# Kernel optimization log

Hardware: AMD Instinct MI355X
Metric: run time of the kernel (lower is better)

The kernel has to match this reference:

```python
import jax, jax.numpy as jnp
import numpy as np

B, S, D, H, F = 16, 1024, 256, 8, 1024
HD = D // H  # head_dim = 32
EPS = 1e-5


def setup_inputs() -> dict:
    key = jax.random.key(0)
    ks = jax.random.split(key, 12)
    sc = 0.02
    return {
        "x":      jax.random.normal(ks[0], (B, S, D), dtype=jnp.float32),
        "gamma1": jnp.ones((S, D), dtype=jnp.float32),
        "beta1":  jnp.zeros((S, D), dtype=jnp.float32),
        "Wqkv":   jax.random.normal(ks[1], (3 * D, D), dtype=jnp.float32) * sc,
        "bqkv":   jnp.zeros((3 * D,), dtype=jnp.float32),
        "Wo":     jax.random.normal(ks[2], (D, D), dtype=jnp.float32) * sc,
        "bo":     jnp.zeros((D,), dtype=jnp.float32),
        "gamma2": jnp.ones((S, D), dtype=jnp.float32),
        "beta2":  jnp.zeros((S, D), dtype=jnp.float32),
        "W1":     jax.random.normal(ks[3], (F, D), dtype=jnp.float32) * sc,
        "b1":     jnp.zeros((F,), dtype=jnp.float32),
        "W2":     jax.random.normal(ks[4], (D, F), dtype=jnp.float32) * sc,
        "b2":     jnp.zeros((D,), dtype=jnp.float32),
    }


def _layernorm_2d(x, gamma, beta):
    # normalizes jointly over the last TWO dims (seq, d_model), biased variance
    mean = jnp.mean(x, axis=(-2, -1), keepdims=True)
    var = jnp.mean((x - mean) ** 2, axis=(-2, -1), keepdims=True)
    y = (x - mean) / jnp.sqrt(var + EPS)
    return gamma * y + beta


def _mha(x, Wqkv, bqkv, Wo, bo):
    b, s, d = x.shape
    qkv = x @ Wqkv.T + bqkv                                  # [B,S,3D]
    qkv = qkv.reshape(b, s, H, 3 * HD).transpose(0, 2, 1, 3)  # [B,H,S,3HD]
    q, k, v = jnp.split(qkv, 3, axis=-1)                      # each [B,H,S,HD]
    scores = jnp.einsum("bhqd,bhkd->bhqk", q, k) / np.sqrt(HD).astype(np.float32)
    attn = jax.nn.softmax(scores, axis=-1)                    # [B,H,S,S]
    values = jnp.einsum("bhqk,bhkd->bhqd", attn, v)           # [B,H,S,HD]
    # NOTE: original torch code reshapes (B,H,S,HD)->(B,S,H*HD) WITHOUT permuting
    # back; we faithfully reproduce that (row-major reshape, same as torch).
    values = values.reshape(b, s, H * HD)
    return values @ Wo.T + bo


def reference(x, gamma1, beta1, Wqkv, bqkv, Wo, bo, gamma2, beta2, W1, b1, W2, b2):
    # pre-norm attention block (dropout is identity at inference)
    h = _layernorm_2d(x, gamma1, beta1)
    h = _mha(h, Wqkv, bqkv, Wo, bo)
    x = x + h
    # pre-norm MLP block
    h = _layernorm_2d(x, gamma2, beta2)
    h = jax.nn.relu(h @ W1.T + b1) @ W2.T + b2
    return x + h
```

## Files before the change

kernel.cpp:

```cpp
#include <hip/hip_runtime.h>
#include <cstdint>
#include <cstddef>

#define SDn (1024*256)

typedef unsigned short u16;
typedef unsigned int   u32;
typedef __bf16 bf16x8 __attribute__((ext_vector_type(8)));
typedef u16    u16x4v __attribute__((ext_vector_type(4)));
typedef u32    u32x4v __attribute__((ext_vector_type(4)));
typedef float  f32x4  __attribute__((ext_vector_type(4)));
typedef float  f32x16 __attribute__((ext_vector_type(16)));

__device__ __forceinline__ u16 f2bf(float f){
  u32 u = __builtin_bit_cast(u32, f);
  u32 r = u + 0x7FFFu + ((u >> 16) & 1u);
  return (u16)(r >> 16);
}

#if __has_builtin(__builtin_amdgcn_exp2f)
#define EXP2(x) __builtin_amdgcn_exp2f(x)
#else
#define EXP2(x) exp2f(x)
#endif

__device__ __forceinline__ u32 cvtpk(float a, float b){
  u32 r;
  asm("v_cvt_pk_bf16_f32 %0, %1, %2" : "=v"(r) : "v"(a), "v"(b));
  return r;
}

__device__ __forceinline__ void gll16(const void* g, void* l){
  __builtin_amdgcn_global_load_lds((const __attribute__((address_space(1))) void*)g,
                                   (__attribute__((address_space(3))) void*)l, 16, 0, 0);
}

__global__ void castw(const float* __restrict__ w0, const float* __restrict__ w1,
                      const float* __restrict__ w2, const float* __restrict__ w3,
                      u16* __restrict__ o0, u16* __restrict__ o1,
                      u16* __restrict__ o2, u16* __restrict__ o3)
{
  int i = blockIdx.x * 256 + threadIdx.x;
  const float* src; u16* dst; int j = i;
  if      (j <  49152){ src = w0; dst = o0; }
  else if (j <  65536){ src = w1; dst = o1; j -=  49152; }
  else if (j < 131072){ src = w2; dst = o2; j -=  65536; }
  else               { src = w3; dst = o3; j -= 131072; }
  float4 v = ((const float4*)src)[j];
  u16x4v o; o[0]=f2bf(v.x); o[1]=f2bf(v.y); o[2]=f2bf(v.z); o[3]=f2bf(v.w);
  ((u16x4v*)dst)[j] = o;
}

__global__ void ln_partial(const float* __restrict__ x, float2* __restrict__ part)
{
  int b = blockIdx.y, c = blockIdx.x, t = threadIdx.x;
  const float4* p = (const float4*)(x + (size_t)b*SDn + (size_t)c*4096);
  float s = 0.f, q = 0.f;
  #pragma unroll
  for (int i=0;i<4;i++){
    float4 v = p[t + i*256];
    s += v.x+v.y+v.z+v.w;
    q += v.x*v.x + v.y*v.y + v.z*v.z + v.w*v.w;
  }
  #pragma unroll
  for (int o=32;o;o>>=1){ s += __shfl_down(s,o); q += __shfl_down(q,o); }
  __shared__ float2 red[4];
  if ((t & 63) == 0) red[t>>6] = make_float2(s,q);
  __syncthreads();
  if (t == 0){
    float S=0.f,Q=0.f;
    #pragma unroll
    for (int i=0;i<4;i++){ S += red[i].x; Q += red[i].y; }
    part[b*64 + c] = make_float2(S,Q);
  }
}

__global__ void ln_apply(const float* __restrict__ x, const float* __restrict__ gamma,
                         const float* __restrict__ beta, const float2* __restrict__ part,
                         u16* __restrict__ y)
{
  int b = blockIdx.y, c = blockIdx.x, t = threadIdx.x;
  __shared__ float2 stat;
  if (t < 64){
    float2 v = part[b*64 + t];
    float s = v.x, q = v.y;
    #pragma unroll
    for (int o=32;o;o>>=1){ s += __shfl_down(s,o); q += __shfl_down(q,o); }
    if (t == 0){
      float mean = s / (float)SDn;
      float var  = q / (float)SDn - mean*mean;
      stat = make_float2(mean, rsqrtf(var + 1e-5f));
    }
  }
  __syncthreads();
  const float mean = stat.x, rstd = stat.y;
  const size_t off = (size_t)b*SDn + (size_t)c*4096;
  const float4* px = (const float4*)(x + off);
  const float4* pg = (const float4*)(gamma + (size_t)c*4096);
  const float4* pb = (const float4*)(beta  + (size_t)c*4096);
  u16x4v* py = (u16x4v*)(y + off);
  #pragma unroll
  for (int i=0;i<4;i++){
    float4 xv = px[t + i*256];
    float4 gv = pg[t + i*256];
    float4 bv = pb[t + i*256];
    u16x4v o;
    o[0] = f2bf(gv.x*(xv.x-mean)*rstd + bv.x);
    o[1] = f2bf(gv.y*(xv.y-mean)*rstd + bv.y);
    o[2] = f2bf(gv.z*(xv.z-mean)*rstd + bv.z);
    o[3] = f2bf(gv.w*(xv.w-mean)*rstd + bv.w);
    py[t + i*256] = o;
  }
}

template<int EPI>
__launch_bounds__(256, 4)
__global__ void gemm128(const u16* __restrict__ A, const u16* __restrict__ W,
                        const float* __restrict__ bias,
                        u16* __restrict__ o0, u16* __restrict__ o1, u16* __restrict__ o2,
                        int K, int N)
{
  __shared__ u16 As[2][4096];
  __shared__ u16 Bs[2][4096];
  const int tid  = threadIdx.x;
  const int lane = tid & 63;
  const int wid  = tid >> 6;
  const int wm = wid >> 1, wn = wid & 1;
  const int g  = lane >> 4;
  const int lr = lane & 15;
  const int m0 = blockIdx.x * 128;
  const int n0 = blockIdx.y * 128;

  f32x4 zf = {0.f,0.f,0.f,0.f};
  f32x4 acc[4][4];
  #pragma unroll
  for (int i=0;i<4;i++)
    #pragma unroll
    for (int j=0;j<4;j++) acc[i][j] = zf;

  const int r0 = tid >> 2, c0 = tid & 3;
  const int cs = c0 ^ ((r0 >> 1) & 3);
  const u16* Ar0 = A + (size_t)(m0 + r0     )*K + cs*8;
  const u16* Ar1 = A + (size_t)(m0 + r0 + 64)*K + cs*8;
  const u16* Wr0 = W + (size_t)(n0 + r0     )*K + cs*8;
  const u16* Wr1 = W + (size_t)(n0 + r0 + 64)*K + cs*8;

  int aoff[4], boff[4];
  #pragma unroll
  for (int m=0;m<4;m++){
    int ra = wm*64 + m*16 + lr;
    aoff[m] = (ra*4 + (g ^ ((ra>>1)&3))) * 8;
    int rb = wn*64 + m*16 + lr;
    boff[m] = (rb*4 + (g ^ ((rb>>1)&3))) * 8;
  }

  auto STAGE = [&](int buf, int k0){
    gll16(Ar0 + k0, &As[buf][tid*8]);
    gll16(Ar1 + k0, &As[buf][(tid+256)*8]);
    gll16(Wr0 + k0, &Bs[buf][tid*8]);
    gll16(Wr1 + k0, &Bs[buf][(tid+256)*8]);
  };

  STAGE(0, 0);
  __syncthreads();
  int cur = 0;
  for (int k0 = 0; k0 < K; k0 += 32){
    if (k0 + 32 < K) STAGE(cur^1, k0 + 32);
    bf16x8 af[4], bfv[4];
    #pragma unroll
    for (int m=0;m<4;m++) af[m]  = *(const bf16x8*)(&As[cur][aoff[m]]);
    #pragma unroll
    for (int n=0;n<4;n++) bfv[n] = *(const bf16x8*)(&Bs[cur][boff[n]]);
    #pragma unroll
    for (int m=0;m<4;m++)
      #pragma unroll
      for (int n=0;n<4;n++)
        acc[m][n] = __builtin_amdgcn_mfma_f32_16x16x32_bf16(af[m], bfv[n], acc[m][n], 0, 0, 0);
    __syncthreads();
    cur ^= 1;
  }

  #pragma unroll
  for (int m=0;m<4;m++){
    const int rowb = m0 + wm*64 + m*16 + g*4;
    #pragma unroll
    for (int n=0;n<4;n++){
      const int col = n0 + wn*64 + n*16 + lr;
      const float bc = bias[col];
      if constexpr (EPI == 0){
        const int hh  = col / 96;
        const int rem = col - hh*96;
        const int which = rem >> 5;
        const int d = rem & 31;
        #pragma unroll
        for (int rr=0;rr<4;rr++){
          const int rw = rowb + rr;
          const int b = rw >> 10, s = rw & 1023;
          float v = acc[m][n][rr] + bc;
          if (which == 0)
            o0[((size_t)((b*8 + hh)*1024 + s))*32 + d] = f2bf(v * (0.17677669529663689f * 1.4426950408889634f));
          else if (which == 1)
            o1[((size_t)((b*8 + hh)*1024 + s))*32 + d] = f2bf(v);
          else
            o2[((size_t)((b*8 + hh)*32 + d))*1024 + s] = f2bf(v);
        }
      } else {
        #pragma unroll
        for (int rr=0;rr<4;rr++){
          float v = acc[m][n][rr] + bc;
          o0[(size_t)(rowb + rr) * N + col] = f2bf(v > 0.f ? v : 0.f);
        }
      }
    }
  }
}

__launch_bounds__(256, 4)
__global__ void gemm64(const u16* __restrict__ A, const u16* __restrict__ W,
                       const float* __restrict__ bias, const float* __restrict__ res,
                       float* __restrict__ outF, int K, int N)
{
  __shared__ u16 As[2][2048];
  __shared__ u16 Bs[2][4096];
  const int tid  = threadIdx.x;
  const int lane = tid & 63;
  const int wid  = tid >> 6;
  const int g  = lane >> 4;
  const int lr = lane & 15;
  const int m0 = blockIdx.x * 64;
  const int n0 = blockIdx.y * 128;

  f32x4 zf = {0.f,0.f,0.f,0.f};
  f32x4 acc[4][2];
  #pragma unroll
  for (int i=0;i<4;i++){ acc[i][0]=zf; acc[i][1]=zf; }

  const int r0 = tid >> 2, c0 = tid & 3;
  const int cs = c0 ^ ((r0 >> 1) & 3);
  const u16* Asrc  = A + (size_t)(m0 + r0)*K + cs*8;
  const u16* Wsrc0 = W + (size_t)(n0 + r0     )*K + cs*8;
  const u16* Wsrc1 = W + (size_t)(n0 + r0 + 64)*K + cs*8;

  int aoff[4], boff[2];
  #pragma unroll
  for (int m=0;m<4;m++){
    int ra = m*16 + lr;
    aoff[m] = (ra*4 + (g ^ ((ra>>1)&3))) * 8;
  }
  #pragma unroll
  for (int n=0;n<2;n++){
    int rb = wid*32 + n*16 + lr;
    boff[n] = (rb*4 + (g ^ ((rb>>1)&3))) * 8;
  }

  auto STAGE = [&](int buf, int k0){
    gll16(Asrc  + k0, &As[buf][tid*8]);
    gll16(Wsrc0 + k0, &Bs[buf][tid*8]);
    gll16(Wsrc1 + k0, &Bs[buf][(tid+256)*8]);
  };

  STAGE(0, 0);
  __syncthreads();
  int cur = 0;
  for (int k0 = 0; k0 < K; k0 += 32){
    if (k0 + 32 < K) STAGE(cur^1, k0 + 32);
    bf16x8 af[4], bfv[2];
    #pragma unroll
    for (int m=0;m<4;m++) af[m]  = *(const bf16x8*)(&As[cur][aoff[m]]);
    #pragma unroll
    for (int n=0;n<2;n++) bfv[n] = *(const bf16x8*)(&Bs[cur][boff[n]]);
    #pragma unroll
    for (int m=0;m<4;m++)
      #pragma unroll
      for (int n=0;n<2;n++)
        acc[m][n] = __builtin_amdgcn_mfma_f32_16x16x32_bf16(af[m], bfv[n], acc[m][n], 0, 0, 0);
    __syncthreads();
    cur ^= 1;
  }

  #pragma unroll
  for (int m=0;m<4;m++){
    const int rowb = m0 + m*16 + g*4;
    #pragma unroll
    for (int n=0;n<2;n++){
      const int col = n0 + wid*32 + n*16 + lr;
      const float bc = bias[col];
      #pragma unroll
      for (int rr=0;rr<4;rr++){
        size_t idx = (size_t)(rowb + rr) * N + col;
        outF[idx] = res[idx] + acc[m][n][rr] + bc;
      }
    }
  }
}

__launch_bounds__(256, 5)
__global__ void attn32(const u16* __restrict__ Q, const u16* __restrict__ Kb,
                       const u16* __restrict__ Vt, u16* __restrict__ vals)
{
  __shared__ u16 Ks[2][4096];
  __shared__ u16 Vs[2][4096];
  const int tid  = threadIdx.x;
  const int lane = tid & 63;
  const int wid  = tid >> 6;
  const int l31  = lane & 31;
  const int l5   = lane >> 5;
  const int bh = blockIdx.x;
  const int q0 = blockIdx.y * 128;
  const size_t base = (size_t)bh * (1024*32);

  const int qrow = q0 + wid*32 + l31;
  const bf16x8 qf0 = *(const bf16x8*)(Q + base + (size_t)qrow*32 + l5*8);
  const bf16x8 qf1 = *(const bf16x8*)(Q + base + (size_t)qrow*32 + 16 + l5*8);

  f32x16 acc = {};
  float lsum = 0.f;

  const int kr = tid >> 2, kc = tid & 3;
  const int vd = tid >> 4, vc = tid & 15;
  const u16* Ksrc0 = Kb + base + (size_t)(kr     )*32 + (kc ^ (kr&3))*8;
  const u16* Ksrc1 = Kb + base + (size_t)(kr + 64)*32 + (kc ^ (kr&3))*8;
  const u16* Vsrc0 = Vt + base + (size_t)(vd     )*1024 + (vc ^ (vd&15))*8;
  const u16* Vsrc1 = Vt + base + (size_t)(vd + 16)*1024 + (vc ^ (vd&15))*8;

  auto STAGE = [&](int buf, int kv0){
    gll16(Ksrc0 + (size_t)kv0*32, &Ks[buf][tid*8]);
    gll16(Ksrc1 + (size_t)kv0*32, &Ks[buf][(tid+256)*8]);
    gll16(Vsrc0 + kv0, &Vs[buf][tid*8]);
    gll16(Vsrc1 + kv0, &Vs[buf][(tid+256)*8]);
  };

  STAGE(0, 0);
  __syncthreads();
  int cur = 0;
  for (int kv0 = 0; kv0 < 1024; kv0 += 128){
    if (kv0 + 128 < 1024) STAGE(cur^1, kv0 + 128);

    #pragma unroll
    for (int G=0; G<4; ++G){
      const u16* ksb = &Ks[cur][(32*G + l31)*32];
      const int sw = l31 & 3;
      bf16x8 kf0 = *(const bf16x8*)(ksb + (((0|l5) ^ sw) << 3));
      bf16x8 kf1 = *(const bf16x8*)(ksb + (((2|l5) ^ sw) << 3));
      f32x16 sf = __builtin_amdgcn_mfma_f32_32x32x16_bf16(kf0, qf0, (f32x16){}, 0, 0, 0);
      sf = __builtin_amdgcn_mfma_f32_32x32x16_bf16(kf1, qf1, sf, 0, 0, 0);

      u32 W[8];
      #pragma unroll
      for (int j=0;j<4;j++){
        float p0 = EXP2(sf[4*j+0]);
        float p1 = EXP2(sf[4*j+1]);
        float p2 = EXP2(sf[4*j+2]);
        float p3 = EXP2(sf[4*j+3]);
        lsum += (p0 + p1) + (p2 + p3);
        W[2*j+0] = cvtpk(p0, p1);
        W[2*j+1] = cvtpk(p2, p3);
      }

      #pragma unroll
      for (int sl=0; sl<2; ++sl){
        u32 a0 = W[4*sl + 0], b0 = W[4*sl + 2];
        u32 a1 = W[4*sl + 1], b1 = W[4*sl + 3];
        asm("v_permlane32_swap_b32 %0, %1" : "+v"(a0), "+v"(b0));
        asm("v_permlane32_swap_b32 %0, %1" : "+v"(a1), "+v"(b1));
        bf16x8 pa = __builtin_bit_cast(bf16x8, (u32x4v){a0, a1, b0, b1});
        const int cp = 4*G + 2*sl + l5;
        bf16x8 vb = *(const bf16x8*)(&Vs[cur][l31*128 + ((cp ^ (l31 & 15)) << 3)]);
        acc = __builtin_amdgcn_mfma_f32_32x32x16_bf16(pa, vb, acc, 0, 0, 0);
      }
    }
    __syncthreads();
    cur ^= 1;
  }

  lsum += __shfl_xor(lsum, 32);
  float inv = 1.0f / lsum;

  const int b = bh >> 3, h = bh & 7;
  #pragma unroll
  for (int r=0;r<16;r++){
    int qloc = (r&3) + 8*(r>>2) + 4*l5;
    float iv = __shfl(inv, qloc);
    int sq = q0 + wid*32 + qloc;
    int srow = h*128 + (sq >> 3);
    vals[((size_t)b*1024 + srow)*256 + (sq&7)*32 + l31] = f2bf(acc[r] * iv);
  }
}

extern "C" void kernel_launch(void* const* d_in, const int* in_sizes, int n_in,
                              void* d_out, int out_size, void* d_ws, size_t ws_size,
                              hipStream_t stream)
{
  const float* x      = (const float*)d_in[0];
  const float* gamma1 = (const float*)d_in[1];
  const float* beta1  = (const float*)d_in[2];
  const float* Wqkv   = (const float*)d_in[3];
  const float* bqkv   = (const float*)d_in[4];
  const float* Wo     = (const float*)d_in[5];
  const float* bo     = (const float*)d_in[6];
  const float* gamma2 = (const float*)d_in[7];
  const float* beta2  = (const float*)d_in[8];
  const float* W1     = (const float*)d_in[9];
  const float* b1     = (const float*)d_in[10];
  const float* W2     = (const float*)d_in[11];
  const float* b2     = (const float*)d_in[12];
  float* out = (float*)d_out;
  char* ws = (char*)d_ws;

  float2* part  = (float2*)(ws + 256);
  u16* wq   = (u16*)(ws + 16384);
  u16* wo   = (u16*)(ws + 409600);
  u16* w1   = (u16*)(ws + 540672);
  u16* w2   = (u16*)(ws + 1064960);
  u16* hbuf = (u16*)(ws + 1589248);
  u16* qb   = (u16*)(ws + 9977856);
  u16* kb   = (u16*)(ws + 18366464);
  u16* vtb  = (u16*)(ws + 26755072);
  u16* valsb= (u16*)(ws + 35143680);
  u16* midb = (u16*)(ws + 9977856);

  castw<<<768, 256, 0, stream>>>(Wqkv, Wo, W1, W2, wq, wo, w1, w2);

  ln_partial<<<dim3(64,16), 256, 0, stream>>>(x, part);
  ln_apply  <<<dim3(64,16), 256, 0, stream>>>(x, gamma1, beta1, part, hbuf);

  gemm128<0><<<dim3(128,6), 256, 0, stream>>>(hbuf, wq, bqkv, qb, kb, vtb, 256, 768);

  attn32<<<dim3(128,8), 256, 0, stream>>>(qb, kb, vtb, valsb);

  gemm64<<<dim3(256,2), 256, 0, stream>>>(valsb, wo, bo, x, out, 256, 256);

  ln_partial<<<dim3(64,16), 256, 0, stream>>>(out, part);
  ln_apply  <<<dim3(64,16), 256, 0, stream>>>(out, gamma2, beta2, part, hbuf);

  gemm128<2><<<dim3(128,8), 256, 0, stream>>>(hbuf, w1, b1, midb, nullptr, nullptr, 256, 1024);

  gemm64<<<dim3(256,2), 256, 0, stream>>>(midb, w2, b2, out, out, 1024, 256);
}
```

Measured before the change: 124.0 us.

## Fuse weight cast with LN1 stats and compute LN2 stats in Wo GEMM epilogue

Merges the weight-cast kernel and the first layernorm partial-stat kernel into one launch. It also moves the second layernorm's sum and sum-of-squares reduction into the Wo projection GEMM epilogue, writing per-block partials that a new ln2_apply kernel reduces. This drops two kernel launches and one full re-read of the residual tensor, at the cost of an extra shuffle reduction and barrier in the GEMM epilogue.

New measurement: 117.0 us. 5.6% less time.

```diff
diff --git a/kernel.cpp b/kernel.cpp
--- a/kernel.cpp
+++ b/kernel.cpp
@@ -35,42 +35,44 @@
                                    (__attribute__((address_space(3))) void*)l, 16, 0, 0);
 }
 
-__global__ void castw(const float* __restrict__ w0, const float* __restrict__ w1,
-                      const float* __restrict__ w2, const float* __restrict__ w3,
-                      u16* __restrict__ o0, u16* __restrict__ o1,
-                      u16* __restrict__ o2, u16* __restrict__ o3)
-{
-  int i = blockIdx.x * 256 + threadIdx.x;
-  const float* src; u16* dst; int j = i;
-  if      (j <  49152){ src = w0; dst = o0; }
-  else if (j <  65536){ src = w1; dst = o1; j -=  49152; }
-  else if (j < 131072){ src = w2; dst = o2; j -=  65536; }
-  else               { src = w3; dst = o3; j -= 131072; }
-  float4 v = ((const float4*)src)[j];
-  u16x4v o; o[0]=f2bf(v.x); o[1]=f2bf(v.y); o[2]=f2bf(v.z); o[3]=f2bf(v.w);
-  ((u16x4v*)dst)[j] = o;
-}
-
-__global__ void ln_partial(const float* __restrict__ x, float2* __restrict__ part)
-{
-  int b = blockIdx.y, c = blockIdx.x, t = threadIdx.x;
+__global__ void prep(const float* __restrict__ x, float2* __restrict__ part,
+                     const float* __restrict__ cw0, const float* __restrict__ cw1,
+                     const float* __restrict__ cw2, const float* __restrict__ cw3,
+                     u16* __restrict__ co0, u16* __restrict__ co1,
+                     u16* __restrict__ co2, u16* __restrict__ co3)
+{
+  const int bid = blockIdx.x, t = threadIdx.x;
+  if (bid < 768){
+    int i = bid*256 + t;
+    const float* src; u16* dst; int j = i;
+    if      (j <  49152){ src = cw0; dst = co0; }
+    else if (j <  65536){ src = cw1; dst = co1; j -=  49152; }
+    else if (j < 131072){ src = cw2; dst = co2; j -=  65536; }
+    else               { src = cw3; dst = co3; j -= 131072; }
+    float4 v = ((const float4*)src)[j];
+    u16x4v o; o[0]=f2bf(v.x); o[1]=f2bf(v.y); o[2]=f2bf(v.z); o[3]=f2bf(v.w);
+    ((u16x4v*)dst)[j] = o;
+    return;
+  }
+  __shared__ float2 red[4];
+  const int i = bid - 768;
+  const int b = i >> 6, c = i & 63;
   const float4* p = (const float4*)(x + (size_t)b*SDn + (size_t)c*4096);
   float s = 0.f, q = 0.f;
   #pragma unroll
-  for (int i=0;i<4;i++){
-    float4 v = p[t + i*256];
+  for (int k=0;k<4;k++){
+    float4 v = p[t + k*256];
     s += v.x+v.y+v.z+v.w;
     q += v.x*v.x + v.y*v.y + v.z*v.z + v.w*v.w;
   }
   #pragma unroll
   for (int o=32;o;o>>=1){ s += __shfl_down(s,o); q += __shfl_down(q,o); }
-  __shared__ float2 red[4];
   if ((t & 63) == 0) red[t>>6] = make_float2(s,q);
   __syncthreads();
   if (t == 0){
     float S=0.f,Q=0.f;
     #pragma unroll
-    for (int i=0;i<4;i++){ S += red[i].x; Q += red[i].y; }
+    for (int k=0;k<4;k++){ S += red[k].x; Q += red[k].y; }
     part[b*64 + c] = make_float2(S,Q);
   }
 }
@@ -86,6 +88,44 @@
     float s = v.x, q = v.y;
     #pragma unroll
     for (int o=32;o;o>>=1){ s += __shfl_down(s,o); q += __shfl_down(q,o); }
+    if (t == 0){
+      float mean = s / (float)SDn;
+      float var  = q / (float)SDn - mean*mean;
+      stat = make_float2(mean, rsqrtf(var + 1e-5f));
+    }
+  }
+  __syncthreads();
+  const float mean = stat.x, rstd = stat.y;
+  const size_t off = (size_t)b*SDn + (size_t)c*4096;
+  const float4* px = (const float4*)(x + off);
+  const float4* pg = (const float4*)(gamma + (size_t)c*4096);
+  const float4* pb = (const float4*)(beta  + (size_t)c*4096);
+  u16x4v* py = (u16x4v*)(y + off);
+  #pragma unroll
+  for (int i=0;i<4;i++){
+    float4 xv = px[t + i*256];
+    float4 gv = pg[t + i*256];
+    float4 bv = pb[t + i*256];
+    u16x4v o;
+    o[0] = f2bf(gv.x*(xv.x-mean)*rstd + bv.x);
+    o[1] = f2bf(gv.y*(xv.y-mean)*rstd + bv.y);
+    o[2] = f2bf(gv.z*(xv.z-mean)*rstd + bv.z);
+    o[3] = f2bf(gv.w*(xv.w-mean)*rstd + bv.w);
+    py[t + i*256] = o;
+  }
+}
+
+__global__ void ln2_apply(const float* __restrict__ x, const float* __restrict__ gamma,
+                          const float* __restrict__ beta, const float2* __restrict__ part2,
+                          u16* __restrict__ y)
+{
+  int b = blockIdx.y, c = blockIdx.x, t = threadIdx.x;
+  __shared__ float2 stat;
+  if (t < 32){
+    float2 v = part2[b*32 + t];
+    float s = v.x, q = v.y;
+    #pragma unroll
+    for (int o=16;o;o>>=1){ s += __shfl_down(s,o); q += __shfl_down(q,o); }
     if (t == 0){
       float mean = s / (float)SDn;
       float var  = q / (float)SDn - mean*mean;
@@ -215,13 +255,16 @@
   }
 }
 
+template<int STATS>
 __launch_bounds__(256, 4)
 __global__ void gemm64(const u16* __restrict__ A, const u16* __restrict__ W,
                        const float* __restrict__ bias, const float* __restrict__ res,
-                       float* __restrict__ outF, int K, int N)
+                       float* __restrict__ outF, float2* __restrict__ part2,
+                       int K, int N)
 {
   __shared__ u16 As[2][2048];
   __shared__ u16 Bs[2][4096];
+  __shared__ float2 sred[4];
   const int tid  = threadIdx.x;
   const int lane = tid & 63;
   const int wid  = tid >> 6;
@@ -278,6 +321,7 @@
     cur ^= 1;
   }
 
+  float s = 0.f, q = 0.f;
   #pragma unroll
   for (int m=0;m<4;m++){
     const int rowb = m0 + m*16 + g*4;
@@ -288,8 +332,23 @@
       #pragma unroll
       for (int rr=0;rr<4;rr++){
         size_t idx = (size_t)(rowb + rr) * N + col;
-        outF[idx] = res[idx] + acc[m][n][rr] + bc;
+        float v = res[idx] + acc[m][n][rr] + bc;
+        outF[idx] = v;
+        if constexpr (STATS){ s += v; q += v*v; }
       }
+    }
+  }
+
+  if constexpr (STATS){
+    #pragma unroll
+    for (int o=32;o;o>>=1){ s += __shfl_down(s,o); q += __shfl_down(q,o); }
+    if (lane == 0) sred[wid] = make_float2(s,q);
+    __syncthreads();
+    if (tid == 0){
+      float S=0.f,Q=0.f;
+      #pragma unroll
+      for (int k=0;k<4;k++){ S += sred[k].x; Q += sred[k].y; }
+      part2[blockIdx.x*2 + blockIdx.y] = make_float2(S,Q);
     }
   }
 }
@@ -408,6 +467,7 @@
   char* ws = (char*)d_ws;
 
   float2* part  = (float2*)(ws + 256);
+  float2* part2 = (float2*)(ws + 12288);
   u16* wq   = (u16*)(ws + 16384);
   u16* wo   = (u16*)(ws + 409600);
   u16* w1   = (u16*)(ws + 540672);
@@ -419,21 +479,19 @@
   u16* valsb= (u16*)(ws + 35143680);
   u16* midb = (u16*)(ws + 9977856);
 
-  castw<<<768, 256, 0, stream>>>(Wqkv, Wo, W1, W2, wq, wo, w1, w2);
-
-  ln_partial<<<dim3(64,16), 256, 0, stream>>>(x, part);
-  ln_apply  <<<dim3(64,16), 256, 0, stream>>>(x, gamma1, beta1, part, hbuf);
+  prep<<<1792, 256, 0, stream>>>(x, part, Wqkv, Wo, W1, W2, wq, wo, w1, w2);
+
+  ln_apply<<<dim3(64,16), 256, 0, stream>>>(x, gamma1, beta1, part, hbuf);
 
   gemm128<0><<<dim3(128,6), 256, 0, stream>>>(hbuf, wq, bqkv, qb, kb, vtb, 256, 768);
 
   attn32<<<dim3(128,8), 256, 0, stream>>>(qb, kb, vtb, valsb);
 
-  gemm64<<<dim3(256,2), 256, 0, stream>>>(valsb, wo, bo, x, out, 256, 256);
-
-  ln_partial<<<dim3(64,16), 256, 0, stream>>>(out, part);
-  ln_apply  <<<dim3(64,16), 256, 0, stream>>>(out, gamma2, beta2, part, hbuf);
+  gemm64<1><<<dim3(256,2), 256, 0, stream>>>(valsb, wo, bo, x, out, part2, 256, 256);
+
+  ln2_apply<<<dim3(64,16), 256, 0, stream>>>(out, gamma2, beta2, part2, hbuf);
 
   gemm128<2><<<dim3(128,8), 256, 0, stream>>>(hbuf, w1, b1, midb, nullptr, nullptr, 256, 1024);
 
-  gemm64<<<dim3(256,2), 256, 0, stream>>>(midb, w2, b2, out, out, 1024, 256);
-}
+  gemm64<0><<<dim3(256,2), 256, 0, stream>>>(midb, w2, b2, out, out, nullptr, 1024, 256);
+}
```
